# Optimization experiments

Measured on AMD Instinct MI355X. Metric: run time of the kernel, lower is better.

Reference implementation:

```python
import jax, jax.numpy as jnp
import numpy as np

B, S, CL, DIM, HEADS, FFN = 2, 2048, 512, 2048, 16, 8192
EPS = 1e-6


def rms_norm(x, w):
    return x * jax.lax.rsqrt(jnp.mean(x * x, axis=-1, keepdims=True) + EPS) * w


def mha(q, k, v, num_heads):
    b, sq, d = q.shape
    sk = k.shape[1]
    hd = d // num_heads
    q = q.reshape(b, sq, num_heads, hd)
    k = k.reshape(b, sk, num_heads, hd)
    v = v.reshape(b, sk, num_heads, hd)
    attn = jnp.einsum('bqhd,bkhd->bhqk', q, k) * (hd ** -0.5)
    attn = jax.nn.softmax(attn, axis=-1)
    out = jnp.einsum('bhqk,bkhd->bqhd', attn, v)
    return out.reshape(b, sq, d)


def setup_inputs() -> dict:
    key = jax.random.key(0)
    ks = iter(jax.random.split(key, 48))
    nrm = lambda shape, scale: jax.random.normal(next(ks), shape, jnp.float32) * scale
    w_scale = DIM ** -0.5
    inp = {
        'x': nrm((B, S, DIM), 1.0),
        'e': nrm((B, 6, DIM), 0.5),
        'context': nrm((B, CL, DIM), 1.0),
        'modulation': nrm((1, 6, DIM), w_scale),
        'norm1_w': jnp.ones((DIM,), jnp.float32),
        'norm2_w': jnp.ones((DIM,), jnp.float32),
        'norm3_w': jnp.ones((DIM,), jnp.float32),
        'sa_nq_w': jnp.ones((DIM,), jnp.float32),
        'sa_nk_w': jnp.ones((DIM,), jnp.float32),
        'ffn_norm_w': jnp.ones((DIM,), jnp.float32),
        'sa_qw': nrm((DIM, DIM), w_scale), 'sa_qb': jnp.zeros((DIM,), jnp.float32),
        'sa_kw': nrm((DIM, DIM), w_scale), 'sa_kb': jnp.zeros((DIM,), jnp.float32),
        'sa_vw': nrm((DIM, DIM), w_scale), 'sa_vb': jnp.zeros((DIM,), jnp.float32),
        'sa_ow': nrm((DIM, DIM), w_scale), 'sa_ob': jnp.zeros((DIM,), jnp.float32),
        'ca_qw': nrm((DIM, DIM), w_scale), 'ca_qb': jnp.zeros((DIM,), jnp.float32),
        'ca_kw': nrm((DIM, DIM), w_scale), 'ca_kb': jnp.zeros((DIM,), jnp.float32),
        'ca_vw': nrm((DIM, DIM), w_scale), 'ca_vb': jnp.zeros((DIM,), jnp.float32),
        'ca_ow': nrm((DIM, DIM), w_scale), 'ca_ob': jnp.zeros((DIM,), jnp.float32),
        'ffn_w1': nrm((DIM, FFN), w_scale), 'ffn_b1': jnp.zeros((FFN,), jnp.float32),
        'ffn_w2': nrm((FFN, DIM), FFN ** -0.5), 'ffn_b2': jnp.zeros((DIM,), jnp.float32),
    }
    return inp


def reference(x, e, context, modulation, norm1_w, norm2_w, norm3_w, sa_nq_w, sa_nk_w,
              ffn_norm_w, sa_qw, sa_qb, sa_kw, sa_kb, sa_vw, sa_vb, sa_ow, sa_ob,
              ca_qw, ca_qb, ca_kw, ca_kb, ca_vw, ca_vb, ca_ow, ca_ob,
              ffn_w1, ffn_b1, ffn_w2, ffn_b2):
    # AdaLN modulation: (modulation + e) chunked into 6 along dim=1 -> each [B,1,DIM]
    mod = modulation + e
    e0, e1, e2, e3, e4, e5 = [mod[:, i:i + 1, :] for i in range(6)]

    # --- self attention with qk_norm=True ---
    h = rms_norm(x, norm1_w) * (1.0 + e1) + e0
    q = rms_norm(h @ sa_qw + sa_qb, sa_nq_w)
    k = rms_norm(h @ sa_kw + sa_kb, sa_nk_w)
    v = h @ sa_vw + sa_vb
    y = mha(q, k, v, HEADS) @ sa_ow + sa_ob
    x = x + y * e2

    # --- cross attention (cross_attn_norm=False, no qk norm) ---
    h = rms_norm(x, norm2_w)
    q = h @ ca_qw + ca_qb
    k = context @ ca_kw + ca_kb
    v = context @ ca_vw + ca_vb
    y = mha(q, k, v, HEADS) @ ca_ow + ca_ob
    x = x + y

    # --- FFN: modulate(norm3(x)) -> RMSNorm -> Linear -> GELU(tanh) -> Linear ---
    h = rms_norm(x, norm3_w) * (1.0 + e4) + e3
    h = rms_norm(h, ffn_norm_w)
    h = jax.nn.gelu(h @ ffn_w1 + ffn_b1, approximate=True)
    y = h @ ffn_w2 + ffn_b2
    x = x + y * e5
    return x
```

## Files before the change

### kernel.cpp

```cpp
#include <hip/hip_runtime.h>
#include <hip/hip_bf16.h>
#include <cstdint>

#define DIM   2048
#define HEADS 16
#define HD    128
#define SEQ   2048
#define CLEN  512
#define FFND  8192
#define BATCH 2

using bf16 = __hip_bfloat16;
typedef __attribute__((ext_vector_type(8))) short  short8;
typedef __attribute__((ext_vector_type(4))) short  short4v;
typedef __attribute__((ext_vector_type(4))) float  f32x4;
typedef __attribute__((ext_vector_type(8))) __bf16 bf16x8;

__device__ __forceinline__ short f2bs(float f){ bf16 h = __float2bfloat16(f); return __builtin_bit_cast(short, h); }
__device__ __forceinline__ float bs2f(short s){ return __builtin_bit_cast(float, (uint32_t)((uint16_t)s) << 16); }

__device__ __forceinline__ f32x4 mfma16(short8 a, short8 b, f32x4 c){
  return __builtin_amdgcn_mfma_f32_16x16x32_bf16(
      __builtin_bit_cast(bf16x8, a), __builtin_bit_cast(bf16x8, b), c, 0, 0, 0);
}

__device__ __forceinline__ void gload_lds16(const void* g, const void* l){
  __builtin_amdgcn_global_load_lds(
      (const __attribute__((address_space(1))) void*)(uintptr_t)g,
      (__attribute__((address_space(3))) void*)(uint32_t)(uintptr_t)l, 16, 0, 0);
}

__device__ __forceinline__ float block_sum(float v, float* sbuf, int tid){
  #pragma unroll
  for (int m = 32; m >= 1; m >>= 1) v += __shfl_xor(v, m, 64);
  const int w = tid >> 6;
  if ((tid & 63) == 0) sbuf[w] = v;
  __syncthreads();
  float r = sbuf[0] + sbuf[1] + sbuf[2] + sbuf[3];
  __syncthreads();
  return r;
}


__global__ void modadd_k(const float* __restrict__ m, const float* __restrict__ e,
                         float* __restrict__ out){
  int i = blockIdx.x * 256 + threadIdx.x;
  out[i] = m[i % (6 * DIM)] + e[i];
}

__global__ void f2b8_k(const float* __restrict__ in, bf16* __restrict__ out){
  int i = blockIdx.x * 256 + threadIdx.x;
  const float4* p = (const float4*)in;
  float4 a = p[2*i], c = p[2*i+1];
  short8 o;
  o[0]=f2bs(a.x); o[1]=f2bs(a.y); o[2]=f2bs(a.z); o[3]=f2bs(a.w);
  o[4]=f2bs(c.x); o[5]=f2bs(c.y); o[6]=f2bs(c.z); o[7]=f2bs(c.w);
  *((short8*)out + i) = o;
}

__global__ __launch_bounds__(256) void transpose_w(const float* __restrict__ W,
                                                   bf16* __restrict__ Wt, int K, int N){
  __shared__ float tile[32][33];
  const int tx = threadIdx.x & 31, ty = threadIdx.x >> 5;
  const size_t k0 = blockIdx.y * 32, n0 = blockIdx.x * 32;
  #pragma unroll
  for (int i = 0; i < 4; i++)
    tile[ty + i*8][tx] = W[(k0 + ty + i*8) * (size_t)N + n0 + tx];
  __syncthreads();
  #pragma unroll
  for (int i = 0; i < 4; i++)
    Wt[(n0 + ty + i*8) * (size_t)K + k0 + tx] = __float2bfloat16(tile[tx][ty + i*8]);
}

template<int MODE>
__global__ __launch_bounds__(256) void norm_x(const float* __restrict__ x,
    const float* __restrict__ w1, const float* __restrict__ w2,
    const float* __restrict__ mod, bf16* __restrict__ out, int S)
{
  const int row = blockIdx.x, tid = threadIdx.x;
  const int b = row / S;
  __shared__ float sbuf[4];
  const float* xr = x + (size_t)row * DIM;
  float v[8];
  #pragma unroll
  for (int i = 0; i < 2; i++){
    float4 t = *(const float4*)(xr + i*1024 + tid*4);
    v[i*4+0]=t.x; v[i*4+1]=t.y; v[i*4+2]=t.z; v[i*4+3]=t.w;
  }
  float ss = 0.f;
  #pragma unroll
  for (int j = 0; j < 8; j++) ss += v[j]*v[j];
  ss = block_sum(ss, sbuf, tid);
  const float r = rsqrtf(ss * (1.0f/DIM) + 1e-6f);
  const float* mb = mod + (size_t)b * 6 * DIM;
  float t8[8];
  #pragma unroll
  for (int i = 0; i < 2; i++)
    #pragma unroll
    for (int j = 0; j < 4; j++){
      int n = i*1024 + tid*4 + j;
      float val = v[i*4+j] * r * w1[n];
      if (MODE == 1) val = val * (1.f + mb[DIM + n]) + mb[n];
      if (MODE == 3) val = val * (1.f + mb[4*DIM + n]) + mb[3*DIM + n];
      t8[i*4+j] = val;
    }
  if (MODE == 3){
    float s2 = 0.f;
    #pragma unroll
    for (int j = 0; j < 8; j++) s2 += t8[j]*t8[j];
    s2 = block_sum(s2, sbuf, tid);
    const float r2 = rsqrtf(s2 * (1.0f/DIM) + 1e-6f);
    #pragma unroll
    for (int i = 0; i < 2; i++)
      #pragma unroll
      for (int j = 0; j < 4; j++){
        int n = i*1024 + tid*4 + j;
        t8[i*4+j] = t8[i*4+j] * r2 * w2[n];
      }
  }
  #pragma unroll
  for (int i = 0; i < 2; i++){
    short4v o;
    #pragma unroll
    for (int j = 0; j < 4; j++) o[j] = f2bs(t8[i*4+j]);
    *(short4v*)(out + (size_t)row*DIM + i*1024 + tid*4) = o;
  }
}

__global__ __launch_bounds__(256) void rmsnorm_bf16_ip(bf16* __restrict__ x,
                                                       const float* __restrict__ w){
  const int row = blockIdx.x, tid = threadIdx.x;
  __shared__ float sbuf[4];
  bf16* xr = x + (size_t)row * DIM;
  short8 v = *(const short8*)(xr + tid*8);
  float f[8]; float ss = 0.f;
  #pragma unroll
  for (int j = 0; j < 8; j++){ f[j] = bs2f(v[j]); ss += f[j]*f[j]; }
  ss = block_sum(ss, sbuf, tid);
  const float r = rsqrtf(ss * (1.0f/DIM) + 1e-6f);
  short8 o;
  #pragma unroll
  for (int j = 0; j < 8; j++) o[j] = f2bs(f[j] * r * w[tid*8 + j]);
  *(short8*)(xr + tid*8) = o;
}

template<int EPI>
__global__ __launch_bounds__(256, 2) void gemm_bf16(
    const bf16* __restrict__ A, const bf16* __restrict__ Bt,
    const float* __restrict__ bias, const float* __restrict__ xin,
    const float* __restrict__ mod, float* __restrict__ outf,
    bf16* __restrict__ outb, int M, int N, int K, int S_tok, int eidx)
{
  __shared__ __align__(16) bf16 lA[128*32];
  __shared__ __align__(16) bf16 lB[128*32];
  const int tid = threadIdx.x;
  const int w = tid >> 6, l = tid & 63;
  const int lrow = l & 15, lhi = l >> 4;
  const int wm = w >> 1, wn = w & 1;
  const size_t m0 = (size_t)blockIdx.y * 128, n0 = (size_t)blockIdx.x * 128;

  f32x4 acc[4][4] = {};

  const int srow = tid >> 2, sseg = tid & 3;
  const bf16* gA = A + (m0 + srow) * (size_t)K + sseg * 8;
  const bf16* gB = Bt + (n0 + srow) * (size_t)K + sseg * 8;
  const bf16* lAp = lA + tid * 8;
  const bf16* lBp = lB + tid * 8;
  const size_t rowskip = (size_t)64 * K;

  for (int k0 = 0; k0 < K; k0 += 32) {
    gload_lds16(gA + k0,           lAp);
    gload_lds16(gA + k0 + rowskip, lAp + 2048);
    gload_lds16(gB + k0,           lBp);
    gload_lds16(gB + k0 + rowskip, lBp + 2048);
    __syncthreads();
    short8 af[4], bfv[4];
    #pragma unroll
    for (int mi = 0; mi < 4; mi++)
      af[mi] = *(const short8*)(lA + (wm*64 + mi*16 + lrow)*32 + lhi*8);
    #pragma unroll
    for (int ni = 0; ni < 4; ni++)
      bfv[ni] = *(const short8*)(lB + (wn*64 + ni*16 + lrow)*32 + lhi*8);
    #pragma unroll
    for (int mi = 0; mi < 4; mi++)
      #pragma unroll
      for (int ni = 0; ni < 4; ni++)
        acc[mi][ni] = mfma16(af[mi], bfv[ni], acc[mi][ni]);
    __syncthreads();
  }

  #pragma unroll
  for (int mi = 0; mi < 4; mi++)
    #pragma unroll
    for (int ni = 0; ni < 4; ni++)
      #pragma unroll
      for (int r = 0; r < 4; r++){
        const size_t m = m0 + wm*64 + mi*16 + lhi*4 + r;
        const size_t n = n0 + wn*64 + ni*16 + lrow;
        float v = acc[mi][ni][r] + bias[n];
        if constexpr (EPI == 0) {
          outb[m * N + n] = __float2bfloat16(v);
        } else if constexpr (EPI == 1) {
          const size_t b = m / S_tok, s = m % S_tok;
          const size_t h = n >> 7, d = n & 127;
          outb[((b*HEADS + h)*HD + d) * S_tok + s] = __float2bfloat16(v);
        } else if constexpr (EPI == 2) {
          const float ev = mod[(m / S_tok) * 6 * DIM + (size_t)eidx * DIM + n];
          outf[m * N + n] = xin[m * N + n] + v * ev;
        } else if constexpr (EPI == 3) {
          outf[m * N + n] += v;
        } else {
          float u = 0.7978845608028654f * (v + 0.044715f * v * v * v);
          outb[m * N + n] = __float2bfloat16(0.5f * v * (1.0f + tanhf(u)));
        }
      }
}

__global__ __launch_bounds__(256, 2) void attn_fwd(
    const bf16* __restrict__ Q, const bf16* __restrict__ Kp, const bf16* __restrict__ Vt,
    bf16* __restrict__ O, int SQ, int SKV)
{
  const int tid = threadIdx.x, w = tid >> 6, l = tid & 63;
  const int lrow = l & 15, lhi = l >> 4;
  const int nwg = gridDim.x;
  const int p = blockIdx.x;
  const int f = (p & 7) * (nwg >> 3) + (p >> 3);
  const int nqb = SQ >> 6;
  const int xq = f % nqb;
  const int h  = (f / nqb) % HEADS;
  const int b  = f / (nqb * HEADS);
  const int q0 = xq * 64 + w * 16;

  __shared__ __align__(16) char kls[2][16384];
  __shared__ __align__(16) char vls[2][16384];
  __shared__ __align__(16) bf16 P[4][16][72];
  const float scale = 0.08838834764831845f;

  const bf16* qp = Q + ((size_t)(b*SQ + q0 + lrow))*DIM + h*HD + lhi*8;
  short8 qf[4];
  #pragma unroll
  for (int ds = 0; ds < 4; ds++) qf[ds] = *(const short8*)(qp + ds*32);

  const bf16* kg = Kp + (size_t)b*SKV*DIM + h*HD;
  const bf16* vg = Vt + (size_t)(b*HEADS + h)*HD*SKV;

  f32x4 acc[8] = {};
  float m_run = -INFINITY, l_run = 0.f;
  const int nt = SKV >> 6;

  auto stage = [&](int buf, int kv0){
    char* kd = &kls[buf][0];
    #pragma unroll
    for (int i = 0; i < 4; i++){
      int sid = i*256 + tid;
      int row = sid >> 4, sg = sid & 15;
      int gsg = sg ^ (row & 7);
      gload_lds16(kg + (size_t)(kv0 + row)*DIM + gsg*8, kd + sid*16);
    }
    char* vd = &vls[buf][0];
    #pragma unroll
    for (int i = 0; i < 4; i++){
      int sid = i*256 + tid;
      int d = sid >> 3, sg = sid & 7;
      int gsg = sg ^ (d & 7);
      gload_lds16(vg + (size_t)d*SKV + kv0 + gsg*8, vd + sid*16);
    }
  };

  stage(0, 0);
  __syncthreads();

  for (int t = 0; t < nt; ++t){
    if (t + 1 < nt) stage((t + 1) & 1, (t + 1) * 64);
    const char* kb = &kls[t & 1][0];
    const char* vb = &vls[t & 1][0];

    f32x4 st[4] = {};
    #pragma unroll
    for (int kvf = 0; kvf < 4; kvf++){
      const int row = kvf*16 + lrow;
      const int rx = row & 7;
      #pragma unroll
      for (int ds = 0; ds < 4; ds++){
        const int seg = (ds*4 + lhi) ^ rx;
        short8 kf = *(const short8*)(kb + row*256 + seg*16);
        st[kvf] = mfma16(kf, qf[ds], st[kvf]);
      }
    }

    float sv[16]; float smax = -INFINITY;
    #pragma unroll
    for (int kvf = 0; kvf < 4; kvf++)
      #pragma unroll
      for (int r = 0; r < 4; r++){
        float xv = st[kvf][r] * scale;
        sv[kvf*4+r] = xv; smax = fmaxf(smax, xv);
      }
    smax = fmaxf(smax, __shfl_xor(smax, 16, 64));
    smax = fmaxf(smax, __shfl_xor(smax, 32, 64));
    const float mnew = fmaxf(m_run, smax);
    const float corr = __expf(m_run - mnew);
    float psum = 0.f;
    #pragma unroll
    for (int i = 0; i < 16; i++){ float pe = __expf(sv[i] - mnew); sv[i] = pe; psum += pe; }
    psum += __shfl_xor(psum, 16, 64); psum += __shfl_xor(psum, 32, 64);
    l_run = l_run * corr + psum;
    m_run = mnew;

    #pragma unroll
    for (int kvf = 0; kvf < 4; kvf++){
      short4v o;
      #pragma unroll
      for (int r = 0; r < 4; r++) o[r] = f2bs(sv[kvf*4+r]);
      *(short4v*)&P[w][lrow][kvf*16 + lhi*4] = o;
    }

    float cr[4];
    #pragma unroll
    for (int r = 0; r < 4; r++) cr[r] = __shfl(corr, lhi*4 + r, 64);
    #pragma unroll
    for (int df = 0; df < 8; df++){
      acc[df][0] *= cr[0]; acc[df][1] *= cr[1]; acc[df][2] *= cr[2]; acc[df][3] *= cr[3];
    }

    asm volatile("s_waitcnt lgkmcnt(0)" ::: "memory");
    __builtin_amdgcn_sched_barrier(0);

    short8 pf0 = *(const short8*)&P[w][lrow][lhi*8];
    short8 pf1 = *(const short8*)&P[w][lrow][32 + lhi*8];
    #pragma unroll
    for (int df = 0; df < 8; df++){
      const int d = df*16 + lrow;
      const int dx = d & 7;
      short8 vf0 = *(const short8*)(vb + d*128 + ((lhi)     ^ dx)*16);
      short8 vf1 = *(const short8*)(vb + d*128 + ((lhi + 4) ^ dx)*16);
      acc[df] = mfma16(pf0, vf0, acc[df]);
      acc[df] = mfma16(pf1, vf1, acc[df]);
    }
    __syncthreads();
  }

  const float linv = 1.0f / l_run;
  float li[4];
  #pragma unroll
  for (int r = 0; r < 4; r++) li[r] = __shfl(linv, lhi*4 + r, 64);
  #pragma unroll
  for (int df = 0; df < 8; df++)
    #pragma unroll
    for (int r = 0; r < 4; r++){
      const size_t q = q0 + lhi*4 + r;
      O[((size_t)(b*SQ + q))*DIM + h*HD + df*16 + lrow] = __float2bfloat16(acc[df][r] * li[r]);
    }
}


extern "C" void kernel_launch(void* const* d_in, const int* in_sizes, int n_in,
                              void* d_out, int out_size, void* d_ws, size_t ws_size,
                              hipStream_t stream)
{
  const float* x    = (const float*)d_in[0];
  const float* e    = (const float*)d_in[1];
  const float* ctx  = (const float*)d_in[2];
  const float* modw = (const float*)d_in[3];
  const float* n1w  = (const float*)d_in[4];
  const float* n2w  = (const float*)d_in[5];
  const float* n3w  = (const float*)d_in[6];
  const float* nqw  = (const float*)d_in[7];
  const float* nkw  = (const float*)d_in[8];
  const float* fnw  = (const float*)d_in[9];
  const float* saqw = (const float*)d_in[10]; const float* saqb = (const float*)d_in[11];
  const float* sakw = (const float*)d_in[12]; const float* sakb = (const float*)d_in[13];
  const float* savw = (const float*)d_in[14]; const float* savb = (const float*)d_in[15];
  const float* saow = (const float*)d_in[16]; const float* saob = (const float*)d_in[17];
  const float* caqw = (const float*)d_in[18]; const float* caqb = (const float*)d_in[19];
  const float* cakw = (const float*)d_in[20]; const float* cakb = (const float*)d_in[21];
  const float* cavw = (const float*)d_in[22]; const float* cavb = (const float*)d_in[23];
  const float* caow = (const float*)d_in[24]; const float* caob = (const float*)d_in[25];
  const float* fw1  = (const float*)d_in[26]; const float* fb1  = (const float*)d_in[27];
  const float* fw2  = (const float*)d_in[28]; const float* fb2  = (const float*)d_in[29];
  float* out = (float*)d_out;
  (void)in_sizes; (void)n_in; (void)out_size; (void)ws_size;

  char* ws = (char*)d_ws;
  size_t off = 0;
  auto alloc = [&](size_t bytes) -> void* {
    void* p = ws + off; off = (off + bytes + 255) & ~(size_t)255; return p;
  };
  bf16*  wt   = (bf16*)alloc((size_t)FFND * DIM * 2);
  float* mod  = (float*)alloc((size_t)BATCH * 6 * DIM * 4);
  bf16*  ctxb = (bf16*)alloc((size_t)BATCH * CLEN * DIM * 2);
  bf16*  hbuf = (bf16*)alloc((size_t)BATCH * SEQ * DIM * 2);
  bf16*  qbuf = (bf16*)alloc((size_t)BATCH * SEQ * DIM * 2);
  bf16*  kbuf = (bf16*)alloc((size_t)BATCH * SEQ * DIM * 2);
  bf16*  vtb  = (bf16*)alloc((size_t)BATCH * SEQ * DIM * 2);
  bf16*  aout = (bf16*)alloc((size_t)BATCH * SEQ * DIM * 2);
  float* xcur = (float*)alloc((size_t)BATCH * SEQ * DIM * 4);
  bf16*  hf   = (bf16*)alloc((size_t)BATCH * SEQ * FFND * 2);

  const int M = BATCH * SEQ;
  const int Mc = BATCH * CLEN;

  modadd_k<<<dim3(96), dim3(256), 0, stream>>>(modw, e, mod);
  f2b8_k<<<dim3(1024), dim3(256), 0, stream>>>(ctx, ctxb);

  norm_x<1><<<dim3(M), dim3(256), 0, stream>>>(x, n1w, nullptr, mod, hbuf, SEQ);

  transpose_w<<<dim3(DIM/32, DIM/32), dim3(256), 0, stream>>>(saqw, wt, DIM, DIM);
  gemm_bf16<0><<<dim3(DIM/128, M/128), dim3(256), 0, stream>>>(hbuf, wt, saqb, nullptr, mod, nullptr, qbuf, M, DIM, DIM, SEQ, 0);
  rmsnorm_bf16_ip<<<dim3(M), dim3(256), 0, stream>>>(qbuf, nqw);

  transpose_w<<<dim3(DIM/32, DIM/32), dim3(256), 0, stream>>>(sakw, wt, DIM, DIM);
  gemm_bf16<0><<<dim3(DIM/128, M/128), dim3(256), 0, stream>>>(hbuf, wt, sakb, nullptr, mod, nullptr, kbuf, M, DIM, DIM, SEQ, 0);
  rmsnorm_bf16_ip<<<dim3(M), dim3(256), 0, stream>>>(kbuf, nkw);

  transpose_w<<<dim3(DIM/32, DIM/32), dim3(256), 0, stream>>>(savw, wt, DIM, DIM);
  gemm_bf16<1><<<dim3(DIM/128, M/128), dim3(256), 0, stream>>>(hbuf, wt, savb, nullptr, mod, nullptr, vtb, M, DIM, DIM, SEQ, 0);

  attn_fwd<<<dim3((SEQ/64)*HEADS*BATCH), dim3(256), 0, stream>>>(qbuf, kbuf, vtb, aout, SEQ, SEQ);

  transpose_w<<<dim3(DIM/32, DIM/32), dim3(256), 0, stream>>>(saow, wt, DIM, DIM);
  gemm_bf16<2><<<dim3(DIM/128, M/128), dim3(256), 0, stream>>>(aout, wt, saob, x, mod, xcur, nullptr, M, DIM, DIM, SEQ, 2);

  norm_x<2><<<dim3(M), dim3(256), 0, stream>>>(xcur, n2w, nullptr, mod, hbuf, SEQ);

  transpose_w<<<dim3(DIM/32, DIM/32), dim3(256), 0, stream>>>(caqw, wt, DIM, DIM);
  gemm_bf16<0><<<dim3(DIM/128, M/128), dim3(256), 0, stream>>>(hbuf, wt, caqb, nullptr, mod, nullptr, qbuf, M, DIM, DIM, SEQ, 0);

  transpose_w<<<dim3(DIM/32, DIM/32), dim3(256), 0, stream>>>(cakw, wt, DIM, DIM);
  gemm_bf16<0><<<dim3(DIM/128, Mc/128), dim3(256), 0, stream>>>(ctxb, wt, cakb, nullptr, mod, nullptr, kbuf, Mc, DIM, DIM, CLEN, 0);

  transpose_w<<<dim3(DIM/32, DIM/32), dim3(256), 0, stream>>>(cavw, wt, DIM, DIM);
  gemm_bf16<1><<<dim3(DIM/128, Mc/128), dim3(256), 0, stream>>>(ctxb, wt, cavb, nullptr, mod, nullptr, vtb, Mc, DIM, DIM, CLEN, 0);

  attn_fwd<<<dim3((SEQ/64)*HEADS*BATCH), dim3(256), 0, stream>>>(qbuf, kbuf, vtb, aout, SEQ, CLEN);

  transpose_w<<<dim3(DIM/32, DIM/32), dim3(256), 0, stream>>>(caow, wt, DIM, DIM);
  gemm_bf16<3><<<dim3(DIM/128, M/128), dim3(256), 0, stream>>>(aout, wt, caob, nullptr, mod, xcur, nullptr, M, DIM, DIM, SEQ, 0);

  norm_x<3><<<dim3(M), dim3(256), 0, stream>>>(xcur, n3w, fnw, mod, hbuf, SEQ);

  transpose_w<<<dim3(FFND/32, DIM/32), dim3(256), 0, stream>>>(fw1, wt, DIM, FFND);
  gemm_bf16<4><<<dim3(FFND/128, M/128), dim3(256), 0, stream>>>(hbuf, wt, fb1, nullptr, mod, nullptr, hf, M, FFND, DIM, SEQ, 0);

  transpose_w<<<dim3(DIM/32, FFND/32), dim3(256), 0, stream>>>(fw2, wt, FFND, DIM);
  gemm_bf16<2><<<dim3(DIM/128, M/128), dim3(256), 0, stream>>>(hf, wt, fb2, xcur, mod, out, nullptr, M, DIM, FFND, SEQ, 5);
}
```

Measured before the change: 1.064 ms.

## Triple-buffer GEMM LDS loads and widen tiles to 128x256 with 8 waves

Replaces the single-buffer, double-sync GEMM main loop with a three-stage LDS ring. Each iteration issues global-to-LDS loads two k-tiles ahead, waits only on the oldest loads with vmcnt, and uses a single barrier per iteration. The block tile grows to 128x256 with 512 threads so A tiles are reused across more columns, and MFMA sections run at raised wave priority. This aims to hide global memory latency and cut barrier stalls, at the cost of more LDS per block (72KB), which may limit occupancy, and fewer blocks for the smaller cross-attention GEMMs.

```diff
diff --git a/kernel.cpp b/kernel.cpp
--- a/kernel.cpp
+++ b/kernel.cpp
@@ -144,49 +144,69 @@
   *(short8*)(xr + tid*8) = o;
 }
 
+#define GBUF 24576
 template<int EPI>
-__global__ __launch_bounds__(256, 2) void gemm_bf16(
+__global__ __launch_bounds__(512, 2) void gemm_bf16(
     const bf16* __restrict__ A, const bf16* __restrict__ Bt,
     const float* __restrict__ bias, const float* __restrict__ xin,
     const float* __restrict__ mod, float* __restrict__ outf,
     bf16* __restrict__ outb, int M, int N, int K, int S_tok, int eidx)
 {
-  __shared__ __align__(16) bf16 lA[128*32];
-  __shared__ __align__(16) bf16 lB[128*32];
+  __shared__ __align__(16) char lds[3][GBUF];
   const int tid = threadIdx.x;
   const int w = tid >> 6, l = tid & 63;
   const int lrow = l & 15, lhi = l >> 4;
-  const int wm = w >> 1, wn = w & 1;
-  const size_t m0 = (size_t)blockIdx.y * 128, n0 = (size_t)blockIdx.x * 128;
+  const int wm = w >> 2, wn = w & 3;
+  const size_t m0 = (size_t)blockIdx.y * 128, n0 = (size_t)blockIdx.x * 256;
 
   f32x4 acc[4][4] = {};
 
   const int srow = tid >> 2, sseg = tid & 3;
-  const bf16* gA = A + (m0 + srow) * (size_t)K + sseg * 8;
+  const bf16* gA = A  + (m0 + srow) * (size_t)K + sseg * 8;
   const bf16* gB = Bt + (n0 + srow) * (size_t)K + sseg * 8;
-  const bf16* lAp = lA + tid * 8;
-  const bf16* lBp = lB + tid * 8;
-  const size_t rowskip = (size_t)64 * K;
-
-  for (int k0 = 0; k0 < K; k0 += 32) {
-    gload_lds16(gA + k0,           lAp);
-    gload_lds16(gA + k0 + rowskip, lAp + 2048);
-    gload_lds16(gB + k0,           lBp);
-    gload_lds16(gB + k0 + rowskip, lBp + 2048);
-    __syncthreads();
-    short8 af[4], bfv[4];
+  const size_t bskip = (size_t)128 * K;
+
+  auto stage = [&](int kt, char* buf){
+    const size_t ko = (size_t)kt * 32;
+    gload_lds16(gA + ko,         buf + tid * 16);
+    gload_lds16(gB + ko,         buf + 8192  + tid * 16);
+    gload_lds16(gB + ko + bskip, buf + 16384 + tid * 16);
+  };
+
+  const int nt = K >> 5;
+  stage(0, lds[0]);
+  stage(1, lds[1]);
+  asm volatile("s_waitcnt vmcnt(3)" ::: "memory");
+  __builtin_amdgcn_s_barrier();
+  __builtin_amdgcn_sched_barrier(0);
+
+  int bi = 0;
+  for (int t = 0; t < nt; ++t){
+    const char* br = lds[bi];
+    const bool st = (t + 2 < nt);
+    if (st){
+      int wi = bi + 2; if (wi >= 3) wi -= 3;
+      stage(t + 2, lds[wi]);
+    }
+    short8 af[4], bf[4];
     #pragma unroll
     for (int mi = 0; mi < 4; mi++)
-      af[mi] = *(const short8*)(lA + (wm*64 + mi*16 + lrow)*32 + lhi*8);
+      af[mi] = *(const short8*)(br + (wm*64 + mi*16 + lrow)*64 + lhi*16);
     #pragma unroll
     for (int ni = 0; ni < 4; ni++)
-      bfv[ni] = *(const short8*)(lB + (wn*64 + ni*16 + lrow)*32 + lhi*8);
+      bf[ni] = *(const short8*)(br + 8192 + (wn*64 + ni*16 + lrow)*64 + lhi*16);
+    __builtin_amdgcn_s_setprio(1);
     #pragma unroll
     for (int mi = 0; mi < 4; mi++)
       #pragma unroll
       for (int ni = 0; ni < 4; ni++)
-        acc[mi][ni] = mfma16(af[mi], bfv[ni], acc[mi][ni]);
-    __syncthreads();
+        acc[mi][ni] = mfma16(af[mi], bf[ni], acc[mi][ni]);
+    __builtin_amdgcn_s_setprio(0);
+    if (st)               { asm volatile("s_waitcnt vmcnt(3)" ::: "memory"); }
+    else if (t + 1 < nt)  { asm volatile("s_waitcnt vmcnt(0)" ::: "memory"); }
+    __builtin_amdgcn_s_barrier();
+    __builtin_amdgcn_sched_barrier(0);
+    bi = (bi + 1 == 3) ? 0 : bi + 1;
   }
 
   #pragma unroll
@@ -406,42 +426,42 @@
   norm_x<1><<<dim3(M), dim3(256), 0, stream>>>(x, n1w, nullptr, mod, hbuf, SEQ);
 
   transpose_w<<<dim3(DIM/32, DIM/32), dim3(256), 0, stream>>>(saqw, wt, DIM, DIM);
-  gemm_bf16<0><<<dim3(DIM/128, M/128), dim3(256), 0, stream>>>(hbuf, wt, saqb, nullptr, mod, nullptr, qbuf, M, DIM, DIM, SEQ, 0);
+  gemm_bf16<0><<<dim3(DIM/256, M/128), dim3(512), 0, stream>>>(hbuf, wt, saqb, nullptr, mod, nullptr, qbuf, M, DIM, DIM, SEQ, 0);
   rmsnorm_bf16_ip<<<dim3(M), dim3(256), 0, stream>>>(qbuf, nqw);
 
   transpose_w<<<dim3(DIM/32, DIM/32), dim3(256), 0, stream>>>(sakw, wt, DIM, DIM);
-  gemm_bf16<0><<<dim3(DIM/128, M/128), dim3(256), 0, stream>>>(hbuf, wt, sakb, nullptr, mod, nullptr, kbuf, M, DIM, DIM, SEQ, 0);
+  gemm_bf16<0><<<dim3(DIM/256, M/128), dim3(512), 0, stream>>>(hbuf, wt, sakb, nullptr, mod, nullptr, kbuf, M, DIM, DIM, SEQ, 0);
   rmsnorm_bf16_ip<<<dim3(M), dim3(256), 0, stream>>>(kbuf, nkw);
 
   transpose_w<<<dim3(DIM/32, DIM/32), dim3(256), 0, stream>>>(savw, wt, DIM, DIM);
-  gemm_bf16<1><<<dim3(DIM/128, M/128), dim3(256), 0, stream>>>(hbuf, wt, savb, nullptr, mod, nullptr, vtb, M, DIM, DIM, SEQ, 0);
+  gemm_bf16<1><<<dim3(DIM/256, M/128), dim3(512), 0, stream>>>(hbuf, wt, savb, nullptr, mod, nullptr, vtb, M, DIM, DIM, SEQ, 0);
 
   attn_fwd<<<dim3((SEQ/64)*HEADS*BATCH), dim3(256), 0, stream>>>(qbuf, kbuf, vtb, aout, SEQ, SEQ);
 
   transpose_w<<<dim3(DIM/32, DIM/32), dim3(256), 0, stream>>>(saow, wt, DIM, DIM);
-  gemm_bf16<2><<<dim3(DIM/128, M/128), dim3(256), 0, stream>>>(aout, wt, saob, x, mod, xcur, nullptr, M, DIM, DIM, SEQ, 2);
+  gemm_bf16<2><<<dim3(DIM/256, M/128), dim3(512), 0, stream>>>(aout, wt, saob, x, mod, xcur, nullptr, M, DIM, DIM, SEQ, 2);
 
   norm_x<2><<<dim3(M), dim3(256), 0, stream>>>(xcur, n2w, nullptr, mod, hbuf, SEQ);
 
   transpose_w<<<dim3(DIM/32, DIM/32), dim3(256), 0, stream>>>(caqw, wt, DIM, DIM);
-  gemm_bf16<0><<<dim3(DIM/128, M/128), dim3(256), 0, stream>>>(hbuf, wt, caqb, nullptr, mod, nullptr, qbuf, M, DIM, DIM, SEQ, 0);
+  gemm_bf16<0><<<dim3(DIM/256, M/128), dim3(512), 0, stream>>>(hbuf, wt, caqb, nullptr, mod, nullptr, qbuf, M, DIM, DIM, SEQ, 0);
 
   transpose_w<<<dim3(DIM/32, DIM/32), dim3(256), 0, stream>>>(cakw, wt, DIM, DIM);
-  gemm_bf16<0><<<dim3(DIM/128, Mc/128), dim3(256), 0, stream>>>(ctxb, wt, cakb, nullptr, mod, nullptr, kbuf, Mc, DIM, DIM, CLEN, 0);
+  gemm_bf16<0><<<dim3(DIM/256, Mc/128), dim3(512), 0, stream>>>(ctxb, wt, cakb, nullptr, mod, nullptr, kbuf, Mc, DIM, DIM, CLEN, 0);
 
   transpose_w<<<dim3(DIM/32, DIM/32), dim3(256), 0, stream>>>(cavw, wt, DIM, DIM);
-  gemm_bf16<1><<<dim3(DIM/128, Mc/128), dim3(256), 0, stream>>>(ctxb, wt, cavb, nullptr, mod, nullptr, vtb, Mc, DIM, DIM, CLEN, 0);
+  gemm_bf16<1><<<dim3(DIM/256, Mc/128), dim3(512), 0, stream>>>(ctxb, wt, cavb, nullptr, mod, nullptr, vtb, Mc, DIM, DIM, CLEN, 0);
 
   attn_fwd<<<dim3((SEQ/64)*HEADS*BATCH), dim3(256), 0, stream>>>(qbuf, kbuf, vtb, aout, SEQ, CLEN);
 
   transpose_w<<<dim3(DIM/32, DIM/32), dim3(256), 0, stream>>>(caow, wt, DIM, DIM);
-  gemm_bf16<3><<<dim3(DIM/128, M/128), dim3(256), 0, stream>>>(aout, wt, caob, nullptr, mod, xcur, nullptr, M, DIM, DIM, SEQ, 0);
+  gemm_bf16<3><<<dim3(DIM/256, M/128), dim3(512), 0, stream>>>(aout, wt, caob, nullptr, mod, xcur, nullptr, M, DIM, DIM, SEQ, 0);
 
   norm_x<3><<<dim3(M), dim3(256), 0, stream>>>(xcur, n3w, fnw, mod, hbuf, SEQ);
 
   transpose_w<<<dim3(FFND/32, DIM/32), dim3(256), 0, stream>>>(fw1, wt, DIM, FFND);
-  gemm_bf16<4><<<dim3(FFND/128, M/128), dim3(256), 0, stream>>>(hbuf, wt, fb1, nullptr, mod, nullptr, hf, M, FFND, DIM, SEQ, 0);
+  gemm_bf16<4><<<dim3(FFND/256, M/128), dim3(512), 0, stream>>>(hbuf, wt, fb1, nullptr, mod, nullptr, hf, M, FFND, DIM, SEQ, 0);
 
   transpose_w<<<dim3(DIM/32, FFND/32), dim3(256), 0, stream>>>(fw2, wt, FFND, DIM);
-  gemm_bf16<2><<<dim3(DIM/128, M/128), dim3(256), 0, stream>>>(hf, wt, fb2, xcur, mod, out, nullptr, M, DIM, FFND, SEQ, 5);
-}
+  gemm_bf16<2><<<dim3(DIM/256, M/128), dim3(512), 0, stream>>>(hf, wt, fb2, xcur, mod, out, nullptr, M, DIM, FFND, SEQ, 5);
+}
```

After: 976.1 us. -8.2%, faster.

## Replace GEMM with double-buffered 256-row tiled kernel and fuse QKV projection

Applied to the files above, without the earlier changes.

Replaces the 128x128 single-buffered GEMM with a 512-thread kernel that uses 256-row tiles, 64-deep K steps, double-buffered LDS, an XOR-swizzled shared-memory layout and prefetch of the next tile overlapped with MFMA work. The self-attention Q, K and V projections are fused into one GEMM over concatenated weights and biases, with a new epilogue that routes output columns to the three buffers. The aim is to cut LDS bank conflicts, hide global-load latency and reduce kernel launches. In exchange it uses more LDS per block, which may lower occupancy, and the cross-attention K/V GEMMs with 1024 rows launch few blocks.

```diff
diff --git a/kernel.cpp b/kernel.cpp
--- a/kernel.cpp
+++ b/kernel.cpp
@@ -56,6 +56,13 @@
   o[0]=f2bs(a.x); o[1]=f2bs(a.y); o[2]=f2bs(a.z); o[3]=f2bs(a.w);
   o[4]=f2bs(c.x); o[5]=f2bs(c.y); o[6]=f2bs(c.z); o[7]=f2bs(c.w);
   *((short8*)out + i) = o;
+}
+
+__global__ void biascat_k(const float* __restrict__ b0, const float* __restrict__ b1,
+                          const float* __restrict__ b2, float* __restrict__ bcat){
+  int i = blockIdx.x * 256 + threadIdx.x;
+  const float* src = (i < DIM) ? b0 : (i < 2*DIM) ? b1 : b2;
+  bcat[i] = src[i & (DIM-1)];
 }
 
 __global__ __launch_bounds__(256) void transpose_w(const float* __restrict__ W,
@@ -144,59 +151,120 @@
   *(short8*)(xr + tid*8) = o;
 }
 
-template<int EPI>
-__global__ __launch_bounds__(256, 2) void gemm_bf16(
+template<int WM, int EPI>
+__global__ __launch_bounds__(512) void gemm_v10(
     const bf16* __restrict__ A, const bf16* __restrict__ Bt,
     const float* __restrict__ bias, const float* __restrict__ xin,
     const float* __restrict__ mod, float* __restrict__ outf,
-    bf16* __restrict__ outb, int M, int N, int K, int S_tok, int eidx)
+    bf16* __restrict__ outb, bf16* __restrict__ out1, bf16* __restrict__ out2,
+    int M, int N, int K, int S_tok, int eidx)
 {
-  __shared__ __align__(16) bf16 lA[128*32];
-  __shared__ __align__(16) bf16 lB[128*32];
+  constexpr int WN  = 8 / WM;
+  constexpr int BN  = WN * 64;
+  constexpr int RPW = 256 / WM;
+  constexpr int MI  = RPW / 16;
+  constexpr int PH  = MI / 2;
+  constexpr int ABYTES = 256 * 64 * 2;
+  constexpr int BBYTES = BN * 64 * 2;
+  constexpr int NBJ = BBYTES / 8192;
+
+  __shared__ __align__(16) char lds[2][ABYTES + BBYTES];
+
   const int tid = threadIdx.x;
   const int w = tid >> 6, l = tid & 63;
   const int lrow = l & 15, lhi = l >> 4;
-  const int wm = w >> 1, wn = w & 1;
-  const size_t m0 = (size_t)blockIdx.y * 128, n0 = (size_t)blockIdx.x * 128;
-
-  f32x4 acc[4][4] = {};
-
-  const int srow = tid >> 2, sseg = tid & 3;
-  const bf16* gA = A + (m0 + srow) * (size_t)K + sseg * 8;
-  const bf16* gB = Bt + (n0 + srow) * (size_t)K + sseg * 8;
-  const bf16* lAp = lA + tid * 8;
-  const bf16* lBp = lB + tid * 8;
-  const size_t rowskip = (size_t)64 * K;
-
-  for (int k0 = 0; k0 < K; k0 += 32) {
-    gload_lds16(gA + k0,           lAp);
-    gload_lds16(gA + k0 + rowskip, lAp + 2048);
-    gload_lds16(gB + k0,           lBp);
-    gload_lds16(gB + k0 + rowskip, lBp + 2048);
-    __syncthreads();
-    short8 af[4], bfv[4];
-    #pragma unroll
-    for (int mi = 0; mi < 4; mi++)
-      af[mi] = *(const short8*)(lA + (wm*64 + mi*16 + lrow)*32 + lhi*8);
+  const int wr = w / WN, wc = w % WN;
+  const size_t m0 = (size_t)blockIdx.y * 256, n0 = (size_t)blockIdx.x * BN;
+
+  f32x4 acc[MI][4] = {};
+
+  const int srow = tid >> 3;
+  const int sseg = (tid & 7) ^ (srow & 7);
+  const bf16* gA[4]; const bf16* gB[NBJ];
+  #pragma unroll
+  for (int j = 0; j < 4; j++)   gA[j] = A  + (m0 + srow + 64*j) * (size_t)K + sseg*8;
+  #pragma unroll
+  for (int j = 0; j < NBJ; j++) gB[j] = Bt + (n0 + srow + 64*j) * (size_t)K + sseg*8;
+
+  const int nt = K >> 6;
+
+  {
+    char* buf = lds[0];
+    #pragma unroll
+    for (int j = 0; j < 4; j++)   gload_lds16(gA[j], buf + (tid + j*512)*16);
+    #pragma unroll
+    for (int j = 0; j < NBJ; j++) gload_lds16(gB[j], buf + ABYTES + (tid + j*512)*16);
+  }
+  asm volatile("s_waitcnt vmcnt(0)" ::: "memory");
+  __builtin_amdgcn_s_barrier();
+
+  for (int t = 0; t < nt; ++t){
+    const char* br = lds[t & 1];
+    char* sb = lds[(t + 1) & 1];
+    const bool dost = (t + 1 < nt);
+    const size_t ko = (size_t)(t + 1) * 64;
+    short8 bf[4];
+    #pragma unroll
+    for (int p = 0; p < PH; ++p){
+      const int ks  = (MI == 8) ? (p >> 1) : p;
+      const int mi0 = (MI == 8) ? (p & 1) * 4 : 0;
+      const int seg = ((ks*4 + lhi) ^ (lrow & 7)) * 16;
+      short8 af[4];
+      #pragma unroll
+      for (int i = 0; i < 4; i++){
+        const int row = wr*RPW + (mi0 + i)*16 + lrow;
+        af[i] = *(const short8*)(br + row*128 + seg);
+      }
+      if (MI == 4 || (p & 1) == 0){
+        #pragma unroll
+        for (int ni = 0; ni < 4; ni++){
+          const int row = wc*64 + ni*16 + lrow;
+          bf[ni] = *(const short8*)(br + ABYTES + row*128 + seg);
+        }
+      }
+      if (dost){
+        if (MI == 8){
+          if (p == 0){
+            #pragma unroll
+            for (int j = 0; j < 4; j++)   gload_lds16(gA[j] + ko, sb + (tid + j*512)*16);
+          } else if (p == 1){
+            #pragma unroll
+            for (int j = 0; j < NBJ; j++) gload_lds16(gB[j] + ko, sb + ABYTES + (tid + j*512)*16);
+          }
+        } else {
+          if (p == 0){
+            #pragma unroll
+            for (int j = 0; j < 4; j++)   gload_lds16(gA[j] + ko, sb + (tid + j*512)*16);
+            #pragma unroll
+            for (int j = 0; j < NBJ; j++) gload_lds16(gB[j] + ko, sb + ABYTES + (tid + j*512)*16);
+          }
+        }
+      }
+      __builtin_amdgcn_sched_barrier(0);
+      __builtin_amdgcn_s_barrier();
+      asm volatile("s_waitcnt lgkmcnt(0)" ::: "memory");
+      __builtin_amdgcn_sched_barrier(0);
+      __builtin_amdgcn_s_setprio(1);
+      #pragma unroll
+      for (int i = 0; i < 4; i++)
+        #pragma unroll
+        for (int ni = 0; ni < 4; ni++)
+          acc[mi0 + i][ni] = mfma16(af[i], bf[ni], acc[mi0 + i][ni]);
+      __builtin_amdgcn_s_setprio(0);
+      if (p == PH - 1){ asm volatile("s_waitcnt vmcnt(0)" ::: "memory"); }
+      __builtin_amdgcn_sched_barrier(0);
+      __builtin_amdgcn_s_barrier();
+    }
+  }
+
+  #pragma unroll
+  for (int mi = 0; mi < MI; mi++)
     #pragma unroll
     for (int ni = 0; ni < 4; ni++)
-      bfv[ni] = *(const short8*)(lB + (wn*64 + ni*16 + lrow)*32 + lhi*8);
-    #pragma unroll
-    for (int mi = 0; mi < 4; mi++)
-      #pragma unroll
-      for (int ni = 0; ni < 4; ni++)
-        acc[mi][ni] = mfma16(af[mi], bfv[ni], acc[mi][ni]);
-    __syncthreads();
-  }
-
-  #pragma unroll
-  for (int mi = 0; mi < 4; mi++)
-    #pragma unroll
-    for (int ni = 0; ni < 4; ni++)
       #pragma unroll
       for (int r = 0; r < 4; r++){
-        const size_t m = m0 + wm*64 + mi*16 + lhi*4 + r;
-        const size_t n = n0 + wn*64 + ni*16 + lrow;
+        const size_t m = m0 + wr*RPW + mi*16 + lhi*4 + r;
+        const size_t n = n0 + wc*64 + ni*16 + lrow;
         float v = acc[mi][ni][r] + bias[n];
         if constexpr (EPI == 0) {
           outb[m * N + n] = __float2bfloat16(v);
@@ -209,9 +277,18 @@
           outf[m * N + n] = xin[m * N + n] + v * ev;
         } else if constexpr (EPI == 3) {
           outf[m * N + n] += v;
-        } else {
+        } else if constexpr (EPI == 4) {
           float u = 0.7978845608028654f * (v + 0.044715f * v * v * v);
           outb[m * N + n] = __float2bfloat16(0.5f * v * (1.0f + tanhf(u)));
+        } else {
+          const size_t sg = n >> 11, col = n & 2047;
+          if (sg == 0)      outb[m * DIM + col] = __float2bfloat16(v);
+          else if (sg == 1) out1[m * DIM + col] = __float2bfloat16(v);
+          else {
+            const size_t b = m / S_tok, s = m % S_tok;
+            const size_t h = col >> 7, d = col & 127;
+            out2[((b*HEADS + h)*HD + d) * S_tok + s] = __float2bfloat16(v);
+          }
         }
       }
 }
@@ -388,6 +465,7 @@
   };
   bf16*  wt   = (bf16*)alloc((size_t)FFND * DIM * 2);
   float* mod  = (float*)alloc((size_t)BATCH * 6 * DIM * 4);
+  float* bcat = (float*)alloc((size_t)3 * DIM * 4);
   bf16*  ctxb = (bf16*)alloc((size_t)BATCH * CLEN * DIM * 2);
   bf16*  hbuf = (bf16*)alloc((size_t)BATCH * SEQ * DIM * 2);
   bf16*  qbuf = (bf16*)alloc((size_t)BATCH * SEQ * DIM * 2);
@@ -402,46 +480,43 @@
 
   modadd_k<<<dim3(96), dim3(256), 0, stream>>>(modw, e, mod);
   f2b8_k<<<dim3(1024), dim3(256), 0, stream>>>(ctx, ctxb);
+  biascat_k<<<dim3(24), dim3(256), 0, stream>>>(saqb, sakb, savb, bcat);
 
   norm_x<1><<<dim3(M), dim3(256), 0, stream>>>(x, n1w, nullptr, mod, hbuf, SEQ);
 
-  transpose_w<<<dim3(DIM/32, DIM/32), dim3(256), 0, stream>>>(saqw, wt, DIM, DIM);
-  gemm_bf16<0><<<dim3(DIM/128, M/128), dim3(256), 0, stream>>>(hbuf, wt, saqb, nullptr, mod, nullptr, qbuf, M, DIM, DIM, SEQ, 0);
+  transpose_w<<<dim3(DIM/32, DIM/32), dim3(256), 0, stream>>>(saqw, wt,                     DIM, DIM);
+  transpose_w<<<dim3(DIM/32, DIM/32), dim3(256), 0, stream>>>(sakw, wt + (size_t)DIM*DIM,   DIM, DIM);
+  transpose_w<<<dim3(DIM/32, DIM/32), dim3(256), 0, stream>>>(savw, wt + (size_t)2*DIM*DIM, DIM, DIM);
+  gemm_v10<2,5><<<dim3(3*DIM/256, M/256), dim3(512), 0, stream>>>(hbuf, wt, bcat, nullptr, nullptr, nullptr, qbuf, kbuf, vtb, M, 3*DIM, DIM, SEQ, 0);
   rmsnorm_bf16_ip<<<dim3(M), dim3(256), 0, stream>>>(qbuf, nqw);
-
-  transpose_w<<<dim3(DIM/32, DIM/32), dim3(256), 0, stream>>>(sakw, wt, DIM, DIM);
-  gemm_bf16<0><<<dim3(DIM/128, M/128), dim3(256), 0, stream>>>(hbuf, wt, sakb, nullptr, mod, nullptr, kbuf, M, DIM, DIM, SEQ, 0);
   rmsnorm_bf16_ip<<<dim3(M), dim3(256), 0, stream>>>(kbuf, nkw);
 
-  transpose_w<<<dim3(DIM/32, DIM/32), dim3(256), 0, stream>>>(savw, wt, DIM, DIM);
-  gemm_bf16<1><<<dim3(DIM/128, M/128), dim3(256), 0, stream>>>(hbuf, wt, savb, nullptr, mod, nullptr, vtb, M, DIM, DIM, SEQ, 0);
-
   attn_fwd<<<dim3((SEQ/64)*HEADS*BATCH), dim3(256), 0, stream>>>(qbuf, kbuf, vtb, aout, SEQ, SEQ);
 
   transpose_w<<<dim3(DIM/32, DIM/32), dim3(256), 0, stream>>>(saow, wt, DIM, DIM);
-  gemm_bf16<2><<<dim3(DIM/128, M/128), dim3(256), 0, stream>>>(aout, wt, saob, x, mod, xcur, nullptr, M, DIM, DIM, SEQ, 2);
+  gemm_v10<4,2><<<dim3(DIM/128, M/256), dim3(512), 0, stream>>>(aout, wt, saob, x, mod, xcur, nullptr, nullptr, nullptr, M, DIM, DIM, SEQ, 2);
 
   norm_x<2><<<dim3(M), dim3(256), 0, stream>>>(xcur, n2w, nullptr, mod, hbuf, SEQ);
 
   transpose_w<<<dim3(DIM/32, DIM/32), dim3(256), 0, stream>>>(caqw, wt, DIM, DIM);
-  gemm_bf16<0><<<dim3(DIM/128, M/128), dim3(256), 0, stream>>>(hbuf, wt, caqb, nullptr, mod, nullptr, qbuf, M, DIM, DIM, SEQ, 0);
+  gemm_v10<4,0><<<dim3(DIM/128, M/256), dim3(512), 0, stream>>>(hbuf, wt, caqb, nullptr, nullptr, nullptr, qbuf, nullptr, nullptr, M, DIM, DIM, SEQ, 0);
 
   transpose_w<<<dim3(DIM/32, DIM/32), dim3(256), 0, stream>>>(cakw, wt, DIM, DIM);
-  gemm_bf16<0><<<dim3(DIM/128, Mc/128), dim3(256), 0, stream>>>(ctxb, wt, cakb, nullptr, mod, nullptr, kbuf, Mc, DIM, DIM, CLEN, 0);
+  gemm_v10<4,0><<<dim3(DIM/128, Mc/256), dim3(512), 0, stream>>>(ctxb, wt, cakb, nullptr, nullptr, nullptr, kbuf, nullptr, nullptr, Mc, DIM, DIM, CLEN, 0);
 
   transpose_w<<<dim3(DIM/32, DIM/32), dim3(256), 0, stream>>>(cavw, wt, DIM, DIM);
-  gemm_bf16<1><<<dim3(DIM/128, Mc/128), dim3(256), 0, stream>>>(ctxb, wt, cavb, nullptr, mod, nullptr, vtb, Mc, DIM, DIM, CLEN, 0);
+  gemm_v10<4,1><<<dim3(DIM/128, Mc/256), dim3(512), 0, stream>>>(ctxb, wt, cavb, nullptr, nullptr, nullptr, vtb, nullptr, nullptr, Mc, DIM, DIM, CLEN, 0);
 
   attn_fwd<<<dim3((SEQ/64)*HEADS*BATCH), dim3(256), 0, stream>>>(qbuf, kbuf, vtb, aout, SEQ, CLEN);
 
   transpose_w<<<dim3(DIM/32, DIM/32), dim3(256), 0, stream>>>(caow, wt, DIM, DIM);
-  gemm_bf16<3><<<dim3(DIM/128, M/128), dim3(256), 0, stream>>>(aout, wt, caob, nullptr, mod, xcur, nullptr, M, DIM, DIM, SEQ, 0);
+  gemm_v10<4,3><<<dim3(DIM/128, M/256), dim3(512), 0, stream>>>(aout, wt, caob, nullptr, nullptr, xcur, nullptr, nullptr, nullptr, M, DIM, DIM, SEQ, 0);
 
   norm_x<3><<<dim3(M), dim3(256), 0, stream>>>(xcur, n3w, fnw, mod, hbuf, SEQ);
 
   transpose_w<<<dim3(FFND/32, DIM/32), dim3(256), 0, stream>>>(fw1, wt, DIM, FFND);
-  gemm_bf16<4><<<dim3(FFND/128, M/128), dim3(256), 0, stream>>>(hbuf, wt, fb1, nullptr, mod, nullptr, hf, M, FFND, DIM, SEQ, 0);
+  gemm_v10<2,4><<<dim3(FFND/256, M/256), dim3(512), 0, stream>>>(hbuf, wt, fb1, nullptr, nullptr, nullptr, hf, nullptr, nullptr, M, FFND, DIM, SEQ, 0);
 
   transpose_w<<<dim3(DIM/32, FFND/32), dim3(256), 0, stream>>>(fw2, wt, FFND, DIM);
-  gemm_bf16<2><<<dim3(DIM/128, M/128), dim3(256), 0, stream>>>(hf, wt, fb2, xcur, mod, out, nullptr, M, DIM, FFND, SEQ, 5);
-}
+  gemm_v10<4,2><<<dim3(DIM/128, M/256), dim3(512), 0, stream>>>(hf, wt, fb2, xcur, mod, out, nullptr, nullptr, nullptr, M, DIM, FFND, SEQ, 5);
+}
```

New measurement: 994.0 us. 1.07x faster.
